# Kernel optimization log

Hardware: AMD Instinct MI355X
Metric: run time of the kernel (lower is better)

## Reference

```python
import jax, jax.numpy as jnp
import numpy as np

B, S, H = 32, 2048, 1024


def setup_inputs() -> dict:
    key = jax.random.key(0)
    k1, k2, k3, k4, k5, k6 = jax.random.split(key, 6)
    scale = 1.0 / np.sqrt(H)
    return {
        "query": jax.random.normal(k1, (B, 1, H), dtype=jnp.float32),
        "encoder_outputs": jax.random.normal(k2, (B, S, H), dtype=jnp.float32),
        "src_lengths": jax.random.randint(k3, (B,), 0, S, dtype=jnp.int64),
        "W_h": jax.random.normal(k4, (H, H), dtype=jnp.float32) * scale,
        "W_s": jax.random.normal(k5, (H, H), dtype=jnp.float32) * scale,
        "v": jax.random.normal(k6, (H,), dtype=jnp.float32) * scale,
    }


def reference(query, encoder_outputs, src_lengths, W_h, W_s, v):
    # score(h_i, s) = v^T tanh(W_h h_i + W_s s)
    proj_h = jnp.einsum("bsh,hd->bsd", encoder_outputs, W_h)   # (B,S,H)
    proj_s = jnp.einsum("bqh,hd->bqd", query, W_s)             # (B,1,H)
    scores = jnp.einsum("bsd,d->bs", jnp.tanh(proj_h + proj_s), v)  # (B,S)
    # sequence mask: True for valid positions
    mask = jnp.arange(encoder_outputs.shape[1])[None, :] < src_lengths[:, None]
    scores = jnp.where(mask, scores, -1e9)
    attn_weights = jax.nn.softmax(scores, axis=1)              # (B,S)
    attn_out = jnp.einsum("bs,bsh->bh", attn_weights, encoder_outputs)
    return attn_out[:, None, :]  # (B,1,H)
```

## Files before the change

### kernel.cpp

```cpp
#include <hip/hip_runtime.h>
#include <hip/hip_bf16.h>
#include <stdint.h>

#define NB 32
#define NS 2048
#define NH 1024

typedef __attribute__((ext_vector_type(8))) unsigned short ushort8v;
typedef __attribute__((ext_vector_type(4))) unsigned short ushort4v;
typedef __attribute__((ext_vector_type(8))) __bf16 bf16x8;
typedef __attribute__((ext_vector_type(4))) float floatx4;

__device__ __forceinline__ unsigned short f2bf(float f) {
    union { float f; unsigned int u; } x; x.f = f;
    unsigned int r = x.u + 0x7fffu + ((x.u >> 16) & 1u);
    return (unsigned short)(r >> 16);
}
__device__ __forceinline__ float bf2f(unsigned short u) {
    union { unsigned int u; float f; } x; x.u = ((unsigned int)u) << 16;
    return x.f;
}
__device__ __forceinline__ float tanh_fast(float x) {
    float e2 = __expf(2.0f * x);
    return 1.0f - 2.0f * __builtin_amdgcn_rcpf(e2 + 1.0f);
}
__device__ __forceinline__ void gload_lds16(const void* g, void* l) {
    __builtin_amdgcn_global_load_lds(
        (const __attribute__((address_space(1))) unsigned int*)g,
        (__attribute__((address_space(3))) unsigned int*)l, 16, 0, 0);
}

__global__ void prep_kernel(const float* __restrict__ E,
                            const int* __restrict__ lens,
                            unsigned short* __restrict__ Ebf,
                            const float* __restrict__ Wh,
                            unsigned short* __restrict__ WhP,
                            const float* __restrict__ q,
                            const float* __restrict__ Ws,
                            float* __restrict__ projs)
{
    const int bid = blockIdx.x;
    const int t   = threadIdx.x;
    if (bid >= 256) {
        int r = bid - 256;
        int len = lens[r >> 11];
        if (len != 0 && (r & (NS - 1)) >= len) return;
        float4 f = *(const float4*)(E + (size_t)r * NH + t * 4);
        ushort4v u;
        u[0] = f2bf(f.x); u[1] = f2bf(f.y); u[2] = f2bf(f.z); u[3] = f2bf(f.w);
        *(ushort4v*)(Ebf + (size_t)r * NH + t * 4) = u;
        return;
    }
    if (bid < 128) {
        int kb = bid;
        int n  = t * 4;
        int ni = n & 15, nh = n >> 4;
        for (int i = 0; i < 8; ++i) {
            int k = kb * 8 + i;
            float4 w = *(const float4*)(Wh + (size_t)k * NH + n);
            size_t base = (size_t)nh * 16384 + (size_t)(k >> 5) * 512 + (k & 31);
            WhP[base + (size_t)(ni + 0) * 32] = f2bf(w.x);
            WhP[base + (size_t)(ni + 1) * 32] = f2bf(w.y);
            WhP[base + (size_t)(ni + 2) * 32] = f2bf(w.z);
            WhP[base + (size_t)(ni + 3) * 32] = f2bf(w.w);
        }
        return;
    }
    {
        int lb = bid - 128;
        int b  = lb >> 2;
        int d0 = (lb & 3) * 256;
        int kg = t >> 6;
        int dc = t & 63;
        const float* qb = q + (size_t)b * NH;
        float4 acc = {0.f, 0.f, 0.f, 0.f};
        for (int k = kg * 256; k < kg * 256 + 256; ++k) {
            float qv = qb[k];
            float4 wv = *(const float4*)(Ws + (size_t)k * NH + d0 + dc * 4);
            acc.x += qv * wv.x; acc.y += qv * wv.y;
            acc.z += qv * wv.z; acc.w += qv * wv.w;
        }
        __shared__ float4 red[4][64];
        red[kg][dc] = acc;
        __syncthreads();
        if (t < 64) {
            float4 s = red[0][t];
            float4 s1 = red[1][t], s2 = red[2][t], s3 = red[3][t];
            s.x += s1.x + s2.x + s3.x; s.y += s1.y + s2.y + s3.y;
            s.z += s1.z + s2.z + s3.z; s.w += s1.w + s2.w + s3.w;
            *(float4*)(projs + (size_t)b * NH + d0 + t * 4) = s;
        }
    }
}

__global__ __launch_bounds__(512) void scores_kernel(
    const unsigned short* __restrict__ Ebf, const unsigned short* __restrict__ WhP,
    const float* __restrict__ projs, const float* __restrict__ v,
    const int* __restrict__ lens, float* __restrict__ spart)
{
    __shared__ __align__(16) unsigned short Al[3][4096];
    __shared__ __align__(16) unsigned short Bl[3][8192];
    __shared__ float sc[4][128];

    const int tid  = threadIdx.x;
    const int wgid = blockIdx.x;
    const int vid  = (wgid & 7) * 256 + (wgid >> 3);
    const int brow = (vid >> 2) * 128;
    const int cb   = vid & 3;
    const int b    = brow >> 11;
    const int sloc = brow & (NS - 1);
    if (sloc >= lens[b]) return;

    const int wave = tid >> 6;
    const int lane = tid & 63;
    const int l15 = lane & 15;
    const int l16 = lane >> 4;
    const int wr = wave >> 2;
    const int wc = wave & 3;

    floatx4 acc[4][4];
    #pragma unroll
    for (int m = 0; m < 4; ++m)
        #pragma unroll
        for (int c = 0; c < 4; ++c) acc[m][c] = (floatx4){0.f, 0.f, 0.f, 0.f};

    const int ssw = ((lane & 3) ^ ((lane >> 3) & 3)) * 8;

    const unsigned short* Asrc = Ebf
        + (size_t)(brow + wave * 16 + (lane >> 2)) * NH + ssw;
    const unsigned short* Bsrc0 = WhP
        + (size_t)(cb * 16 + wave * 2) * 16384 + (lane >> 2) * 32 + ssw;
    const unsigned short* Bsrc1 = Bsrc0 + 16384;

    #define STAGE(buf, kc)                                                     \
    {                                                                          \
        gload_lds16(Asrc + (size_t)(kc) * 32, (void*)&Al[buf][wave * 512]);    \
        gload_lds16(Bsrc0 + (size_t)(kc) * 512, (void*)&Bl[buf][(wave * 2) * 512]); \
        gload_lds16(Bsrc1 + (size_t)(kc) * 512, (void*)&Bl[buf][(wave * 2 + 1) * 512]); \
    }

    const int aslot = (l16 ^ ((l15 >> 1) & 3)) * 8;
    const int bslot = aslot;

    #define COMPUTE(buf)                                                       \
    {                                                                          \
        bf16x8 a[4], bfr[4];                                                   \
        _Pragma("unroll")                                                      \
        for (int m = 0; m < 4; ++m)                                            \
            a[m] = __builtin_bit_cast(bf16x8, *(const ushort8v*)               \
                &Al[buf][(wr * 64 + m * 16 + l15) * 32 + aslot]);              \
        _Pragma("unroll")                                                      \
        for (int c = 0; c < 4; ++c)                                            \
            bfr[c] = __builtin_bit_cast(bf16x8, *(const ushort8v*)             \
                &Bl[buf][(wc * 4 + c) * 512 + l15 * 32 + bslot]);              \
        __builtin_amdgcn_s_setprio(1);                                         \
        _Pragma("unroll")                                                      \
        for (int m = 0; m < 4; ++m)                                            \
            _Pragma("unroll")                                                  \
            for (int c = 0; c < 4; ++c)                                        \
                acc[m][c] = __builtin_amdgcn_mfma_f32_16x16x32_bf16(           \
                    a[m], bfr[c], acc[m][c], 0, 0, 0);                         \
        __builtin_amdgcn_s_setprio(0);                                         \
    }

    STAGE(0, 0);

    for (int kc = 0; kc < 31; ++kc) {
        const int rbuf = kc % 3;
        const int sbuf = (kc + 1) % 3;
        STAGE(sbuf, kc + 1);
        asm volatile("s_waitcnt vmcnt(3)" ::: "memory");
        __builtin_amdgcn_sched_barrier(0);
        __builtin_amdgcn_s_barrier();
        COMPUTE(rbuf);
    }
    asm volatile("s_waitcnt vmcnt(0)" ::: "memory");
    __builtin_amdgcn_sched_barrier(0);
    __builtin_amdgcn_s_barrier();
    COMPUTE(31 % 3);
    #undef STAGE
    #undef COMPUTE

    float psv[4], vv[4];
    #pragma unroll
    for (int c = 0; c < 4; ++c) {
        int col = cb * 256 + wc * 64 + c * 16 + l15;
        psv[c] = projs[(size_t)b * NH + col];
        vv[c]  = v[col];
    }
    #pragma unroll
    for (int m = 0; m < 4; ++m) {
        float sp[4] = {0.f, 0.f, 0.f, 0.f};
        #pragma unroll
        for (int c = 0; c < 4; ++c)
            #pragma unroll
            for (int i2 = 0; i2 < 4; ++i2)
                sp[i2] += tanh_fast(acc[m][c][i2] + psv[c]) * vv[c];
        #pragma unroll
        for (int i2 = 0; i2 < 4; ++i2) {
            float s = sp[i2];
            s += __shfl_xor(s, 1);
            s += __shfl_xor(s, 2);
            s += __shfl_xor(s, 4);
            s += __shfl_xor(s, 8);
            if (l15 == 0) sc[wc][wr * 64 + m * 16 + l16 * 4 + i2] = s;
        }
    }
    __syncthreads();
    if (tid < 128) {
        float s = sc[0][tid] + sc[1][tid] + sc[2][tid] + sc[3][tid];
        spart[(size_t)cb * (NB * NS) + brow + tid] = s;
    }
}

__global__ void attnout1_kernel(const unsigned short* __restrict__ Ebf,
                                const float* __restrict__ spart,
                                const int* __restrict__ lens,
                                float* __restrict__ part)
{
    int b  = blockIdx.x;
    int ch = blockIdx.y;
    int s0 = ch * 128;
    int t  = threadIdx.x;
    int len = lens[b];
    float* po = part + ((size_t)ch * NB + b) * NH;
    if (len > 0 && s0 >= len) {
        *(float4*)(po + t * 4) = (float4){0.f, 0.f, 0.f, 0.f};
        return;
    }
    const float* p0 = spart + (size_t)b * NS;
    float loc[8];
    float mx = -3e38f;
    #pragma unroll
    for (int i = 0; i < 8; ++i) {
        int s = t + i * 256;
        float val = -1e9f;
        if (s < len) {
            val = 0.f;
            #pragma unroll
            for (int c = 0; c < 4; ++c) val += p0[(size_t)c * (NB * NS) + s];
        }
        loc[i] = val;
        mx = fmaxf(mx, val);
    }
    #pragma unroll
    for (int m = 32; m >= 1; m >>= 1) mx = fmaxf(mx, __shfl_xor(mx, m));
    __shared__ float red[4], red2[4];
    __shared__ float wsh[128];
    int w = t >> 6;
    if ((t & 63) == 0) red[w] = mx;
    __syncthreads();
    mx = fmaxf(fmaxf(red[0], red[1]), fmaxf(red[2], red[3]));
    float sum = 0.f;
    #pragma unroll
    for (int i = 0; i < 8; ++i) sum += expf(loc[i] - mx);
    #pragma unroll
    for (int m = 32; m >= 1; m >>= 1) sum += __shfl_xor(sum, m);
    if ((t & 63) == 0) red2[w] = sum;
    __syncthreads();
    sum = red2[0] + red2[1] + red2[2] + red2[3];
    float inv = 1.f / sum;
    if (t < 128) {
        int s = s0 + t;
        float val = -1e9f;
        if (s < len) {
            val = 0.f;
            #pragma unroll
            for (int c = 0; c < 4; ++c) val += p0[(size_t)c * (NB * NS) + s];
        }
        wsh[t] = expf(val - mx) * inv;
    }
    __syncthreads();
    int h0 = t * 4;
    const unsigned short* Eb = Ebf + ((size_t)b * NS + s0) * NH + h0;
    float4 acc = {0.f, 0.f, 0.f, 0.f};
    for (int s = 0; s < 128; ++s) {
        float wv = wsh[s];
        ushort4v e = *(const ushort4v*)(Eb + (size_t)s * NH);
        acc.x += wv * bf2f(e[0]); acc.y += wv * bf2f(e[1]);
        acc.z += wv * bf2f(e[2]); acc.w += wv * bf2f(e[3]);
    }
    *(float4*)(po + h0) = acc;
}

__global__ void attnout2_kernel(const float* __restrict__ part,
                                float* __restrict__ out)
{
    int b = blockIdx.x, t = threadIdx.x;
    float4 acc = {0.f, 0.f, 0.f, 0.f};
    #pragma unroll
    for (int c = 0; c < 16; ++c) {
        float4 p = *(const float4*)(part + ((size_t)c * NB + b) * NH + t * 4);
        acc.x += p.x; acc.y += p.y; acc.z += p.z; acc.w += p.w;
    }
    *(float4*)(out + (size_t)b * NH + t * 4) = acc;
}

extern "C" void kernel_launch(void* const* d_in, const int* in_sizes, int n_in,
                              void* d_out, int out_size, void* d_ws, size_t ws_size,
                              hipStream_t stream)
{
    const float* q    = (const float*)d_in[0];
    const float* E    = (const float*)d_in[1];
    const int*   lens = (const int*)d_in[2];
    const float* Wh   = (const float*)d_in[3];
    const float* Ws   = (const float*)d_in[4];
    const float* v    = (const float*)d_in[5];
    float* out = (float*)d_out;

    float* ws     = (float*)d_ws;
    float* projs  = ws;
    float* spart  = projs + 32 * 1024;
    float* part   = spart + 4 * NB * NS;
    unsigned short* WhP = (unsigned short*)(part + 16 * NB * NH);
    unsigned short* Ebf = WhP + 1024 * 1024;

    prep_kernel    <<<256 + NB * NS, 256, 0, stream>>>(E, lens, Ebf, Wh, WhP, q, Ws, projs);
    scores_kernel  <<<2048, 512, 0, stream>>>(Ebf, WhP, projs, v, lens, spart);
    attnout1_kernel<<<dim3(NB, 16), 256, 0, stream>>>(Ebf, spart, lens, part);
    attnout2_kernel<<<NB, 256, 0, stream>>>(part, out);
}
```

Measured before the change: 148.6 us.

## Enlarge scores GEMM tile to 256 rows with 64-deep K and double buffering

The scores GEMM tile doubles from 128 to 256 rows and the K step from 32 to 64. Each wave now holds an 8x4 grid of MFMA accumulators, and the kernel uses dynamic shared memory (132 KB) with double buffering in place of triple buffering. The aim is to raise arithmetic intensity per tile and halve the number of workgroups, which cuts redundant W_h loads and barrier overhead. In exchange it uses more registers and LDS, so occupancy is lower, and each K step waits on vmcnt(0), which may expose load latency.

```diff
diff --git a/kernel.cpp b/kernel.cpp
--- a/kernel.cpp
+++ b/kernel.cpp
@@ -98,15 +98,17 @@
     const float* __restrict__ projs, const float* __restrict__ v,
     const int* __restrict__ lens, float* __restrict__ spart)
 {
-    __shared__ __align__(16) unsigned short Al[3][4096];
-    __shared__ __align__(16) unsigned short Bl[3][8192];
-    __shared__ float sc[4][128];
+    extern __shared__ __align__(16) unsigned short smem[];
+    unsigned short* Al = smem;
+    unsigned short* Bl = smem + 32768;
+    float* sc = (float*)(smem + 65536);
 
     const int tid  = threadIdx.x;
     const int wgid = blockIdx.x;
-    const int vid  = (wgid & 7) * 256 + (wgid >> 3);
-    const int brow = (vid >> 2) * 128;
+    const int vid  = (wgid & 7) * 128 + (wgid >> 3);
+    const int rt   = vid >> 2;
     const int cb   = vid & 3;
+    const int brow = rt * 256;
     const int b    = brow >> 11;
     const int sloc = brow & (NS - 1);
     if (sloc >= lens[b]) return;
@@ -115,100 +117,107 @@
     const int lane = tid & 63;
     const int l15 = lane & 15;
     const int l16 = lane >> 4;
-    const int wr = wave >> 2;
-    const int wc = wave & 3;
-
-    floatx4 acc[4][4];
-    #pragma unroll
-    for (int m = 0; m < 4; ++m)
+    const int wM = wave >> 2;
+    const int wN = wave & 3;
+
+    floatx4 acc[8][4];
+    #pragma unroll
+    for (int m = 0; m < 8; ++m)
         #pragma unroll
-        for (int c = 0; c < 4; ++c) acc[m][c] = (floatx4){0.f, 0.f, 0.f, 0.f};
-
-    const int ssw = ((lane & 3) ^ ((lane >> 3) & 3)) * 8;
-
-    const unsigned short* Asrc = Ebf
-        + (size_t)(brow + wave * 16 + (lane >> 2)) * NH + ssw;
-    const unsigned short* Bsrc0 = WhP
-        + (size_t)(cb * 16 + wave * 2) * 16384 + (lane >> 2) * 32 + ssw;
-    const unsigned short* Bsrc1 = Bsrc0 + 16384;
-
-    #define STAGE(buf, kc)                                                     \
+        for (int n = 0; n < 4; ++n) acc[m][n] = (floatx4){0.f, 0.f, 0.f, 0.f};
+
+    const unsigned short* AsrcB = Ebf
+        + (size_t)(brow + wave * 32 + (lane >> 3)) * NH
+        + ((lane & 7) ^ (lane >> 3)) * 8;
+    const unsigned short* BsrcB = WhP
+        + (size_t)(cb * 16 + wave * 2) * 16384
+        + (lane >> 2) * 32 + ((lane & 3) ^ ((lane >> 3) & 3)) * 8;
+
+    #define STAGE(buf, kt)                                                     \
     {                                                                          \
-        gload_lds16(Asrc + (size_t)(kc) * 32, (void*)&Al[buf][wave * 512]);    \
-        gload_lds16(Bsrc0 + (size_t)(kc) * 512, (void*)&Bl[buf][(wave * 2) * 512]); \
-        gload_lds16(Bsrc1 + (size_t)(kc) * 512, (void*)&Bl[buf][(wave * 2 + 1) * 512]); \
-    }
-
-    const int aslot = (l16 ^ ((l15 >> 1) & 3)) * 8;
-    const int bslot = aslot;
-
-    #define COMPUTE(buf)                                                       \
+        _Pragma("unroll")                                                      \
+        for (int u = 0; u < 4; ++u)                                            \
+            gload_lds16(AsrcB + (size_t)(u * 8) * NH + (kt) * 64,              \
+                        (void*)&Al[(buf) * 16384 + (wave * 4 + u) * 512]);     \
+        _Pragma("unroll")                                                      \
+        for (int u = 0; u < 4; ++u)                                            \
+            gload_lds16(BsrcB + (size_t)(u >> 1) * 16384                       \
+                              + ((kt) * 2 + (u & 1)) * 512,                    \
+                        (void*)&Bl[(buf) * 16384 + (wave * 4 + u) * 512]);     \
+    }
+
+    const int arow = wM * 128 + l15;
+    const int asw7 = l15 & 7;
+    const int bsw = (l16 ^ ((l15 >> 1) & 3)) * 8;
+
+    #define PHASE(buf, kk)                                                     \
     {                                                                          \
-        bf16x8 a[4], bfr[4];                                                   \
-        _Pragma("unroll")                                                      \
-        for (int m = 0; m < 4; ++m)                                            \
+        bf16x8 a[8]; bf16x8 bb[4];                                             \
+        _Pragma("unroll")                                                      \
+        for (int m = 0; m < 8; ++m)                                            \
             a[m] = __builtin_bit_cast(bf16x8, *(const ushort8v*)               \
-                &Al[buf][(wr * 64 + m * 16 + l15) * 32 + aslot]);              \
-        _Pragma("unroll")                                                      \
-        for (int c = 0; c < 4; ++c)                                            \
-            bfr[c] = __builtin_bit_cast(bf16x8, *(const ushort8v*)             \
-                &Bl[buf][(wc * 4 + c) * 512 + l15 * 32 + bslot]);              \
+                &Al[(buf) * 16384 + (arow + m * 16) * 64                       \
+                    + (((kk) * 4 + l16) ^ asw7) * 8]);                         \
+        _Pragma("unroll")                                                      \
+        for (int n = 0; n < 4; ++n)                                            \
+            bb[n] = __builtin_bit_cast(bf16x8, *(const ushort8v*)              \
+                &Bl[(buf) * 16384 + ((wN * 4 + n) * 2 + (kk)) * 512            \
+                    + l15 * 32 + bsw]);                                        \
         __builtin_amdgcn_s_setprio(1);                                         \
         _Pragma("unroll")                                                      \
-        for (int m = 0; m < 4; ++m)                                            \
+        for (int m = 0; m < 8; ++m)                                            \
             _Pragma("unroll")                                                  \
-            for (int c = 0; c < 4; ++c)                                        \
-                acc[m][c] = __builtin_amdgcn_mfma_f32_16x16x32_bf16(           \
-                    a[m], bfr[c], acc[m][c], 0, 0, 0);                         \
+            for (int n = 0; n < 4; ++n)                                        \
+                acc[m][n] = __builtin_amdgcn_mfma_f32_16x16x32_bf16(           \
+                    a[m], bb[n], acc[m][n], 0, 0, 0);                          \
         __builtin_amdgcn_s_setprio(0);                                         \
     }
 
     STAGE(0, 0);
 
-    for (int kc = 0; kc < 31; ++kc) {
-        const int rbuf = kc % 3;
-        const int sbuf = (kc + 1) % 3;
-        STAGE(sbuf, kc + 1);
-        asm volatile("s_waitcnt vmcnt(3)" ::: "memory");
+    for (int kt = 0; kt < 16; ++kt) {
+        const int buf = kt & 1;
+        asm volatile("s_waitcnt vmcnt(0)" ::: "memory");
         __builtin_amdgcn_sched_barrier(0);
         __builtin_amdgcn_s_barrier();
-        COMPUTE(rbuf);
-    }
-    asm volatile("s_waitcnt vmcnt(0)" ::: "memory");
-    __builtin_amdgcn_sched_barrier(0);
-    __builtin_amdgcn_s_barrier();
-    COMPUTE(31 % 3);
+        __builtin_amdgcn_sched_barrier(0);
+        if (kt < 15) STAGE(buf ^ 1, kt + 1);
+        PHASE(buf, 0);
+        __builtin_amdgcn_s_barrier();
+        __builtin_amdgcn_sched_barrier(0);
+        PHASE(buf, 1);
+    }
     #undef STAGE
-    #undef COMPUTE
+    #undef PHASE
 
     float psv[4], vv[4];
     #pragma unroll
-    for (int c = 0; c < 4; ++c) {
-        int col = cb * 256 + wc * 64 + c * 16 + l15;
-        psv[c] = projs[(size_t)b * NH + col];
-        vv[c]  = v[col];
-    }
-    #pragma unroll
-    for (int m = 0; m < 4; ++m) {
+    for (int n = 0; n < 4; ++n) {
+        int col = cb * 256 + wN * 64 + n * 16 + l15;
+        psv[n] = projs[(size_t)b * NH + col];
+        vv[n]  = v[col];
+    }
+    #pragma unroll
+    for (int m = 0; m < 8; ++m) {
         float sp[4] = {0.f, 0.f, 0.f, 0.f};
         #pragma unroll
-        for (int c = 0; c < 4; ++c)
+        for (int n = 0; n < 4; ++n)
             #pragma unroll
-            for (int i2 = 0; i2 < 4; ++i2)
-                sp[i2] += tanh_fast(acc[m][c][i2] + psv[c]) * vv[c];
+            for (int i = 0; i < 4; ++i)
+                sp[i] += tanh_fast(acc[m][n][i] + psv[n]) * vv[n];
         #pragma unroll
-        for (int i2 = 0; i2 < 4; ++i2) {
-            float s = sp[i2];
+        for (int i = 0; i < 4; ++i) {
+            float s = sp[i];
             s += __shfl_xor(s, 1);
             s += __shfl_xor(s, 2);
             s += __shfl_xor(s, 4);
             s += __shfl_xor(s, 8);
-            if (l15 == 0) sc[wc][wr * 64 + m * 16 + l16 * 4 + i2] = s;
+            if (l15 == 0) sc[wN * 256 + wM * 128 + m * 16 + l16 * 4 + i] = s;
         }
     }
     __syncthreads();
-    if (tid < 128) {
-        float s = sc[0][tid] + sc[1][tid] + sc[2][tid] + sc[3][tid];
+    if (tid < 256) {
+        float s = sc[tid] + sc[256 + tid] + sc[512 + tid] + sc[768 + tid];
         spart[(size_t)cb * (NB * NS) + brow + tid] = s;
     }
 }
@@ -315,8 +324,12 @@
     unsigned short* WhP = (unsigned short*)(part + 16 * NB * NH);
     unsigned short* Ebf = WhP + 1024 * 1024;
 
+    const int smem_bytes = 132 * 1024;
+    hipFuncSetAttribute((const void*)scores_kernel,
+                        hipFuncAttributeMaxDynamicSharedMemorySize, smem_bytes);
+
     prep_kernel    <<<256 + NB * NS, 256, 0, stream>>>(E, lens, Ebf, Wh, WhP, q, Ws, projs);
-    scores_kernel  <<<2048, 512, 0, stream>>>(Ebf, WhP, projs, v, lens, spart);
+    scores_kernel  <<<1024, 512, smem_bytes, stream>>>(Ebf, WhP, projs, v, lens, spart);
     attnout1_kernel<<<dim3(NB, 16), 256, 0, stream>>>(Ebf, spart, lens, part);
     attnout2_kernel<<<NB, 256, 0, stream>>>(part, out);
 }
```

New measurement: 152.9 us. +2.9%, slower.
